# Optimization experiments

Hardware: AMD Instinct MI355X
Metric: run time of the kernel (lower is better)

The kernel has to match this reference:

```python
import jax, jax.numpy as jnp
import numpy as np

MAX_PAIRS = 130816  # = L*(L-1)//2 for L=512; matches init max_pairs


def setup_inputs() -> dict:
    key = jax.random.key(0)
    k1, k2, k3, k4, k5 = jax.random.split(key, 5)
    B, L, H = 32, 512, 1024
    hidden_states = jax.random.normal(k1, (B, L, H), dtype=jnp.float32)
    attention_mask = jax.random.randint(k2, (B, L), 0, 2, dtype=jnp.int32)
    special_tokens_mask = jax.random.randint(k3, (B, L), 0, 2, dtype=jnp.int32)
    # nn.Bilinear(H, H, 1): weight (1, H, H) -> squeeze to (H, H); bias (1,)
    bound = 1.0 / np.sqrt(H)
    W = jax.random.uniform(k4, (H, H), dtype=jnp.float32, minval=-bound, maxval=bound)
    b = jax.random.uniform(k5, (1,), dtype=jnp.float32, minval=-bound, maxval=bound)
    return {"hidden_states": hidden_states, "attention_mask": attention_mask,
            "special_tokens_mask": special_tokens_mask, "W": W, "b": b}


def reference(hidden_states, attention_mask, special_tokens_mask, W, b):
    # Dropout is identity in eval mode (reference assumes inference math).
    B, L, H = hidden_states.shape
    m = (attention_mask == 1) & (special_tokens_mask == 0)  # (B, L) valid AA positions

    # Bilinear score for every (t, s) pair: S[b,t,s] = h_t^T W h_s + bias
    u = jnp.einsum('blh,hk->blk', hidden_states, W)          # (B, L, H)
    S = jnp.einsum('blk,bmk->blm', u, hidden_states) + b[0]  # (B, L, L)

    # Compacted rank of each valid position (order-preserving, like nonzero()).
    r = jnp.cumsum(m.astype(jnp.int32), axis=-1) - 1          # (B, L)
    n = jnp.sum(m.astype(jnp.int32), axis=-1)[:, None, None]  # (B, 1, 1) = n_aa

    pos = jnp.arange(L, dtype=jnp.int32)
    # pair valid iff both positions are AA and t < s (compacted order preserves original order)
    valid = m[:, :, None] & m[:, None, :] & (pos[:, None] < pos[None, :])  # (B, L, L)

    i = r[:, :, None]  # compacted row index (B, L, 1)
    j = r[:, None, :]  # compacted col index (B, 1, L)
    # row-major upper-triangle (offset=1) linear index, matching torch.triu_indices order
    idx = i * (n - 1) - (i * (i - 1)) // 2 + (j - i - 1)
    idx = jnp.where(valid, idx, MAX_PAIRS)  # invalid pairs -> dump slot

    def scatter_one(s_row, ix_row):
        out = jnp.zeros((MAX_PAIRS + 1,), dtype=s_row.dtype)
        out = out.at[ix_row.reshape(-1)].set(s_row.reshape(-1))
        return out[:MAX_PAIRS]

    return jax.vmap(scatter_one)(S, idx)  # (B, MAX_PAIRS)
```

## Files before the change

### kernel.cpp

```cpp
#include <hip/hip_runtime.h>

constexpr int NB   = 32;
constexpr int LL   = 512;
constexpr int HH   = 1024;
constexpr int MAXP = 130816;
constexpr int RMAX = 256;

typedef __attribute__((ext_vector_type(8))) short short8;
typedef __attribute__((ext_vector_type(4))) float f32x4;

static __device__ inline unsigned short f2bf(float f) {
    unsigned int u = __float_as_uint(f);
    unsigned int r = (u + 0x7FFFu + ((u >> 16) & 1u)) >> 16;
    return (unsigned short)r;
}

#define GLOAD16(g, l) __builtin_amdgcn_global_load_lds( \
    (const __attribute__((address_space(1))) unsigned int*)(g), \
    (__attribute__((address_space(3))) unsigned int*)(l), 16, 0, 0)

__global__ __launch_bounds__(512) void prep1_kernel(
        const int* __restrict__ am, const int* __restrict__ sm,
        int* __restrict__ pos, int* __restrict__ ncnt,
        float4* __restrict__ out4, int n4) {
    if (blockIdx.x < NB) {
        int b = blockIdx.x;
        int t = threadIdx.x;
        bool m = (am[b * LL + t] == 1) && (sm[b * LL + t] == 0);
        unsigned long long bal = __ballot(m);
        int lane = t & 63;
        int w = t >> 6;
        __shared__ int wtot[8];
        if (lane == 0) wtot[w] = __popcll(bal);
        pos[b * LL + t] = 0;
        __syncthreads();
        int off = 0;
        for (int i = 0; i < w; ++i) off += wtot[i];
        int pre = __popcll(bal & ((1ULL << lane) - 1ULL));
        int r = off + pre;
        if (t == LL - 1) {
            int tot = 0;
            for (int i = 0; i < 8; ++i) tot += wtot[i];
            ncnt[b] = tot;
        }
        if (m) pos[b * LL + r] = t;
    } else {
        int i = (blockIdx.x - NB) * 512 + threadIdx.x;
        int stride = (gridDim.x - NB) * 512;
        float4 z = {0.f, 0.f, 0.f, 0.f};
        for (; i < n4; i += stride) out4[i] = z;
    }
}

__global__ __launch_bounds__(256) void prep2_kernel(
        const float* __restrict__ W, unsigned short* __restrict__ wt,
        const float* __restrict__ hs, const int* __restrict__ pos,
        const int* __restrict__ ncnt, unsigned short* __restrict__ hc) {
    if (blockIdx.x < 256) {
        __shared__ float T[64][65];
        int th = blockIdx.x >> 4, tj = blockIdx.x & 15;
        int t = threadIdx.x;
        int r0 = t >> 4, c4 = (t & 15) * 4;
        #pragma unroll
        for (int q = 0; q < 4; ++q) {
            int r = r0 + q * 16;
            float4 v = *(const float4*)(W + (size_t)(th * 64 + r) * HH + tj * 64 + c4);
            T[r][c4] = v.x; T[r][c4 + 1] = v.y; T[r][c4 + 2] = v.z; T[r][c4 + 3] = v.w;
        }
        __syncthreads();
        #pragma unroll
        for (int q = 0; q < 4; ++q) {
            int r = r0 + q * 16;
            ushort4 o;
            o.x = f2bf(T[c4 + 0][r]);
            o.y = f2bf(T[c4 + 1][r]);
            o.z = f2bf(T[c4 + 2][r]);
            o.w = f2bf(T[c4 + 3][r]);
            *(ushort4*)(wt + (size_t)(tj * 64 + r) * HH + th * 64 + c4) = o;
        }
    } else {
        int bi = blockIdx.x - 256;
        int b = bi >> 8, i = bi & 255;
        int n = min(ncnt[b], RMAX);
        int npad = min(RMAX, (n + 127) & ~127);
        if (i >= npad) return;
        int t = threadIdx.x;
        ushort4 o; o.x = 0; o.y = 0; o.z = 0; o.w = 0;
        if (i < n) {
            int g = pos[b * LL + i];
            float4 v = *(const float4*)(hs + ((size_t)b * LL + g) * HH + t * 4);
            o.x = f2bf(v.x); o.y = f2bf(v.y); o.z = f2bf(v.z); o.w = f2bf(v.w);
        }
        *(ushort4*)(hc + ((size_t)b * RMAX + i) * HH + t * 4) = o;
    }
}

__global__ __launch_bounds__(256) void gemm1_kernel(
        const unsigned short* __restrict__ hc, const unsigned short* __restrict__ wt,
        const int* __restrict__ ncnt, unsigned short* __restrict__ uc) {
    constexpr int BK = 64;
    int b = blockIdx.z;
    int n = min(ncnt[b], RMAX);
    int it = blockIdx.y;
    if (it * 64 >= n) return;
    int kt = blockIdx.x;

    __shared__ unsigned short As[64 * BK];
    __shared__ unsigned short Bs[64 * BK];

    int tid = threadIdx.x;
    int lane = tid & 63, w = tid >> 6, wr = w >> 1, wc = w & 1;

    const unsigned short* ga = hc + ((size_t)b * RMAX + it * 64) * HH;
    const unsigned short* gb = wt + (size_t)kt * 64 * HH;

    int f0 = tid, f1 = tid + 256;
    int r0 = f0 >> 3, r1 = f1 >> 3;
    int so0 = ((f0 & 7) ^ (r0 & 7)) * 8;
    int so1 = ((f1 & 7) ^ (r1 & 7)) * 8;

    f32x4 acc[2][2];
    #pragma unroll
    for (int m = 0; m < 2; ++m)
        #pragma unroll
        for (int nn = 0; nn < 2; ++nn) { acc[m][nn].x = 0.f; acc[m][nn].y = 0.f; acc[m][nn].z = 0.f; acc[m][nn].w = 0.f; }

    int fr = lane & 15;
    int khi = (lane >> 4) * 8;

    for (int k0 = 0; k0 < HH; k0 += BK) {
        GLOAD16(ga + (size_t)r0 * HH + k0 + so0, As + f0 * 8);
        GLOAD16(ga + (size_t)r1 * HH + k0 + so1, As + f1 * 8);
        GLOAD16(gb + (size_t)r0 * HH + k0 + so0, Bs + f0 * 8);
        GLOAD16(gb + (size_t)r1 * HH + k0 + so1, Bs + f1 * 8);
        __syncthreads();

        #pragma unroll
        for (int ks = 0; ks < 2; ++ks) {
            int k8 = ks * 32 + khi;
            short8 a[2], bb[2];
            #pragma unroll
            for (int m = 0; m < 2; ++m) {
                int row = wr * 32 + m * 16 + fr;
                a[m] = *(const short8*)&As[row * BK + (k8 ^ ((row & 7) * 8))];
            }
            #pragma unroll
            for (int nn = 0; nn < 2; ++nn) {
                int row = wc * 32 + nn * 16 + fr;
                bb[nn] = *(const short8*)&Bs[row * BK + (k8 ^ ((row & 7) * 8))];
            }
            #pragma unroll
            for (int m = 0; m < 2; ++m)
                #pragma unroll
                for (int nn = 0; nn < 2; ++nn)
                    acc[m][nn] = __builtin_amdgcn_mfma_f32_16x16x32_bf16(a[m], bb[nn], acc[m][nn], 0, 0, 0);
        }
        __syncthreads();
    }

    int rowb = it * 64 + wr * 32 + (lane >> 4) * 4;
    int colb = kt * 64 + wc * 32 + (lane & 15);
    #pragma unroll
    for (int m = 0; m < 2; ++m)
        #pragma unroll
        for (int nn = 0; nn < 2; ++nn)
            #pragma unroll
            for (int r = 0; r < 4; ++r)
                uc[((size_t)b * RMAX + rowb + m * 16 + r) * HH + colb + nn * 16] = f2bf(acc[m][nn][r]);
}

__global__ __launch_bounds__(256) void gemm2_kernel(
        const unsigned short* __restrict__ uc, const unsigned short* __restrict__ hc,
        const int* __restrict__ ncnt, const float* __restrict__ bias_p,
        float* __restrict__ out) {
    constexpr int BK = 64;
    int b = blockIdx.z;
    int it = blockIdx.y, jt = blockIdx.x;
    if (jt < it) return;
    int n = min(ncnt[b], RMAX);
    if (it * 64 >= n || jt * 64 >= n) return;

    __shared__ unsigned short Us[64 * BK];
    __shared__ unsigned short Hs[64 * BK];

    int tid = threadIdx.x;
    int lane = tid & 63, w = tid >> 6, wr = w >> 1, wc = w & 1;

    const unsigned short* ga = uc + ((size_t)b * RMAX + it * 64) * HH;
    const unsigned short* gb = hc + ((size_t)b * RMAX + jt * 64) * HH;

    int f0 = tid, f1 = tid + 256;
    int r0 = f0 >> 3, r1 = f1 >> 3;
    int so0 = ((f0 & 7) ^ (r0 & 7)) * 8;
    int so1 = ((f1 & 7) ^ (r1 & 7)) * 8;

    f32x4 acc[2][2];
    #pragma unroll
    for (int m = 0; m < 2; ++m)
        #pragma unroll
        for (int nn = 0; nn < 2; ++nn) { acc[m][nn].x = 0.f; acc[m][nn].y = 0.f; acc[m][nn].z = 0.f; acc[m][nn].w = 0.f; }

    int fr = lane & 15;
    int khi = (lane >> 4) * 8;

    for (int k0 = 0; k0 < HH; k0 += BK) {
        GLOAD16(ga + (size_t)r0 * HH + k0 + so0, Us + f0 * 8);
        GLOAD16(ga + (size_t)r1 * HH + k0 + so1, Us + f1 * 8);
        GLOAD16(gb + (size_t)r0 * HH + k0 + so0, Hs + f0 * 8);
        GLOAD16(gb + (size_t)r1 * HH + k0 + so1, Hs + f1 * 8);
        __syncthreads();

        #pragma unroll
        for (int ks = 0; ks < 2; ++ks) {
            int k8 = ks * 32 + khi;
            short8 a[2], bb[2];
            #pragma unroll
            for (int m = 0; m < 2; ++m) {
                int row = wr * 32 + m * 16 + fr;
                a[m] = *(const short8*)&Us[row * BK + (k8 ^ ((row & 7) * 8))];
            }
            #pragma unroll
            for (int nn = 0; nn < 2; ++nn) {
                int row = wc * 32 + nn * 16 + fr;
                bb[nn] = *(const short8*)&Hs[row * BK + (k8 ^ ((row & 7) * 8))];
            }
            #pragma unroll
            for (int m = 0; m < 2; ++m)
                #pragma unroll
                for (int nn = 0; nn < 2; ++nn)
                    acc[m][nn] = __builtin_amdgcn_mfma_f32_16x16x32_bf16(a[m], bb[nn], acc[m][nn], 0, 0, 0);
        }
        __syncthreads();
    }

    float bias = bias_p[0];
    #pragma unroll
    for (int m = 0; m < 2; ++m)
        #pragma unroll
        for (int nn = 0; nn < 2; ++nn)
            #pragma unroll
            for (int r = 0; r < 4; ++r) {
                int i = it * 64 + wr * 32 + m * 16 + (lane >> 4) * 4 + r;
                int j = jt * 64 + wc * 32 + nn * 16 + (lane & 15);
                if (i < j && j < n) {
                    int idx = i * (n - 1) - (i * (i - 1)) / 2 + (j - i - 1);
                    out[(size_t)b * MAXP + idx] = acc[m][nn][r] + bias;
                }
            }
}

extern "C" void kernel_launch(void* const* d_in, const int* in_sizes, int n_in,
                              void* d_out, int out_size, void* d_ws, size_t ws_size,
                              hipStream_t stream) {
    const float* hs  = (const float*)d_in[0];
    const int*   am  = (const int*)d_in[1];
    const int*   sm  = (const int*)d_in[2];
    const float* W   = (const float*)d_in[3];
    const float* bp  = (const float*)d_in[4];
    float* out = (float*)d_out;

    char* ws = (char*)d_ws;
    int* pos  = (int*)ws;
    int* ncnt = (int*)(ws + NB * LL * 4);
    unsigned short* hc = (unsigned short*)(ws + NB * LL * 4 + 256);
    unsigned short* wt = hc + (size_t)NB * RMAX * HH;
    unsigned short* uc = wt + (size_t)HH * HH;

    prep1_kernel<<<NB + 1024, 512, 0, stream>>>(am, sm, pos, ncnt,
                                                (float4*)out, (NB * MAXP) / 4);
    prep2_kernel<<<256 + NB * RMAX, 256, 0, stream>>>(W, wt, hs, pos, ncnt, hc);
    gemm1_kernel<<<dim3(HH / 64, RMAX / 64, NB), 256, 0, stream>>>(hc, wt, ncnt, uc);
    gemm2_kernel<<<dim3(RMAX / 64, RMAX / 64, NB), 256, 0, stream>>>(uc, hc, ncnt, bp, out);
}
```

Before: 56.65 us.

## Merge W transpose into prep kernel, widen gemm1 N-tile, trim gather padding

Moves the W transpose/bf16 conversion into the first prep kernel alongside mask compaction and output zeroing, and enlarges the zeroing grid. The gather becomes its own kernel with padding to multiples of 64 instead of 128, which skips some zero rows. gemm1 now uses a 64x128 tile with 8 accumulators per wave for more B reuse, and its grid order is swapped so the row tiles vary fastest. Address computation is hoisted out of the k-loops and f2bf is replaced with the library conversion. The larger tile raises register and LDS use, and the changed grid shape gives fewer blocks.

```diff
diff --git a/kernel.cpp b/kernel.cpp
--- a/kernel.cpp
+++ b/kernel.cpp
@@ -1,4 +1,5 @@
 #include <hip/hip_runtime.h>
+#include <hip/hip_bf16.h>
 
 constexpr int NB   = 32;
 constexpr int LL   = 512;
@@ -10,21 +11,23 @@
 typedef __attribute__((ext_vector_type(4))) float f32x4;
 
 static __device__ inline unsigned short f2bf(float f) {
-    unsigned int u = __float_as_uint(f);
-    unsigned int r = (u + 0x7FFFu + ((u >> 16) & 1u)) >> 16;
-    return (unsigned short)r;
+    __hip_bfloat16 h = __float2bfloat16(f);
+    union { __hip_bfloat16 h; unsigned short u; } cv; cv.h = h;
+    return cv.u;
 }
 
 #define GLOAD16(g, l) __builtin_amdgcn_global_load_lds( \
     (const __attribute__((address_space(1))) unsigned int*)(g), \
     (__attribute__((address_space(3))) unsigned int*)(l), 16, 0, 0)
 
-__global__ __launch_bounds__(512) void prep1_kernel(
+__global__ __launch_bounds__(512) void prep_kernel(
         const int* __restrict__ am, const int* __restrict__ sm,
         int* __restrict__ pos, int* __restrict__ ncnt,
+        const float* __restrict__ W, unsigned short* __restrict__ wt,
         float4* __restrict__ out4, int n4) {
-    if (blockIdx.x < NB) {
-        int b = blockIdx.x;
+    int bi = blockIdx.x;
+    if (bi < NB) {
+        int b = bi;
         int t = threadIdx.x;
         bool m = (am[b * LL + t] == 1) && (sm[b * LL + t] == 0);
         unsigned long long bal = __ballot(m);
@@ -44,55 +47,49 @@
             ncnt[b] = tot;
         }
         if (m) pos[b * LL + r] = t;
+    } else if (bi < NB + 256) {
+        __shared__ float T[64][65];
+        int tile = bi - NB;
+        int th = tile >> 4, tj = tile & 15;
+        int t = threadIdx.x;
+        int r = t >> 3;
+        int c8 = (t & 7) * 8;
+        float4 v0 = *(const float4*)(W + (size_t)(th * 64 + r) * HH + tj * 64 + c8);
+        float4 v1 = *(const float4*)(W + (size_t)(th * 64 + r) * HH + tj * 64 + c8 + 4);
+        T[r][c8 + 0] = v0.x; T[r][c8 + 1] = v0.y; T[r][c8 + 2] = v0.z; T[r][c8 + 3] = v0.w;
+        T[r][c8 + 4] = v1.x; T[r][c8 + 5] = v1.y; T[r][c8 + 6] = v1.z; T[r][c8 + 7] = v1.w;
+        __syncthreads();
+        ushort4 o0, o1;
+        o0.x = f2bf(T[c8 + 0][r]); o0.y = f2bf(T[c8 + 1][r]);
+        o0.z = f2bf(T[c8 + 2][r]); o0.w = f2bf(T[c8 + 3][r]);
+        o1.x = f2bf(T[c8 + 4][r]); o1.y = f2bf(T[c8 + 5][r]);
+        o1.z = f2bf(T[c8 + 6][r]); o1.w = f2bf(T[c8 + 7][r]);
+        unsigned short* dst = wt + (size_t)(tj * 64 + r) * HH + th * 64 + c8;
+        *(ushort4*)dst = o0;
+        *(ushort4*)(dst + 4) = o1;
     } else {
-        int i = (blockIdx.x - NB) * 512 + threadIdx.x;
-        int stride = (gridDim.x - NB) * 512;
+        int i = (bi - NB - 256) * 512 + threadIdx.x;
+        int stride = (gridDim.x - NB - 256) * 512;
         float4 z = {0.f, 0.f, 0.f, 0.f};
         for (; i < n4; i += stride) out4[i] = z;
     }
 }
 
-__global__ __launch_bounds__(256) void prep2_kernel(
-        const float* __restrict__ W, unsigned short* __restrict__ wt,
+__global__ __launch_bounds__(256) void gather_kernel(
         const float* __restrict__ hs, const int* __restrict__ pos,
         const int* __restrict__ ncnt, unsigned short* __restrict__ hc) {
-    if (blockIdx.x < 256) {
-        __shared__ float T[64][65];
-        int th = blockIdx.x >> 4, tj = blockIdx.x & 15;
-        int t = threadIdx.x;
-        int r0 = t >> 4, c4 = (t & 15) * 4;
-        #pragma unroll
-        for (int q = 0; q < 4; ++q) {
-            int r = r0 + q * 16;
-            float4 v = *(const float4*)(W + (size_t)(th * 64 + r) * HH + tj * 64 + c4);
-            T[r][c4] = v.x; T[r][c4 + 1] = v.y; T[r][c4 + 2] = v.z; T[r][c4 + 3] = v.w;
-        }
-        __syncthreads();
-        #pragma unroll
-        for (int q = 0; q < 4; ++q) {
-            int r = r0 + q * 16;
-            ushort4 o;
-            o.x = f2bf(T[c4 + 0][r]);
-            o.y = f2bf(T[c4 + 1][r]);
-            o.z = f2bf(T[c4 + 2][r]);
-            o.w = f2bf(T[c4 + 3][r]);
-            *(ushort4*)(wt + (size_t)(tj * 64 + r) * HH + th * 64 + c4) = o;
-        }
-    } else {
-        int bi = blockIdx.x - 256;
-        int b = bi >> 8, i = bi & 255;
-        int n = min(ncnt[b], RMAX);
-        int npad = min(RMAX, (n + 127) & ~127);
-        if (i >= npad) return;
-        int t = threadIdx.x;
-        ushort4 o; o.x = 0; o.y = 0; o.z = 0; o.w = 0;
-        if (i < n) {
-            int g = pos[b * LL + i];
-            float4 v = *(const float4*)(hs + ((size_t)b * LL + g) * HH + t * 4);
-            o.x = f2bf(v.x); o.y = f2bf(v.y); o.z = f2bf(v.z); o.w = f2bf(v.w);
-        }
-        *(ushort4*)(hc + ((size_t)b * RMAX + i) * HH + t * 4) = o;
-    }
+    int b = blockIdx.y, i = blockIdx.x;
+    int n = min(ncnt[b], RMAX);
+    int npad = min(RMAX, (n + 63) & ~63);
+    if (i >= npad) return;
+    int t = threadIdx.x;
+    ushort4 o; o.x = 0; o.y = 0; o.z = 0; o.w = 0;
+    if (i < n) {
+        int g = pos[b * LL + i];
+        float4 v = *(const float4*)(hs + ((size_t)b * LL + g) * HH + t * 4);
+        o.x = f2bf(v.x); o.y = f2bf(v.y); o.z = f2bf(v.z); o.w = f2bf(v.w);
+    }
+    *(ushort4*)(hc + ((size_t)b * RMAX + i) * HH + t * 4) = o;
 }
 
 __global__ __launch_bounds__(256) void gemm1_kernel(
@@ -101,69 +98,78 @@
     constexpr int BK = 64;
     int b = blockIdx.z;
     int n = min(ncnt[b], RMAX);
-    int it = blockIdx.y;
+    int it = blockIdx.x;
     if (it * 64 >= n) return;
-    int kt = blockIdx.x;
+    int kt = blockIdx.y;
 
     __shared__ unsigned short As[64 * BK];
-    __shared__ unsigned short Bs[64 * BK];
+    __shared__ unsigned short Bs[128 * BK];
 
     int tid = threadIdx.x;
     int lane = tid & 63, w = tid >> 6, wr = w >> 1, wc = w & 1;
 
     const unsigned short* ga = hc + ((size_t)b * RMAX + it * 64) * HH;
-    const unsigned short* gb = wt + (size_t)kt * 64 * HH;
-
-    int f0 = tid, f1 = tid + 256;
-    int r0 = f0 >> 3, r1 = f1 >> 3;
-    int so0 = ((f0 & 7) ^ (r0 & 7)) * 8;
-    int so1 = ((f1 & 7) ^ (r1 & 7)) * 8;
-
-    f32x4 acc[2][2];
-    #pragma unroll
-    for (int m = 0; m < 2; ++m)
-        #pragma unroll
-        for (int nn = 0; nn < 2; ++nn) { acc[m][nn].x = 0.f; acc[m][nn].y = 0.f; acc[m][nn].z = 0.f; acc[m][nn].w = 0.f; }
+    const unsigned short* gb = wt + (size_t)kt * 128 * HH;
+
+    int fa0 = tid, fa1 = tid + 256;
+    int ar0 = fa0 >> 3, ar1 = fa1 >> 3;
+    const unsigned short* gar0 = ga + (size_t)ar0 * HH + ((fa0 & 7) ^ (ar0 & 7)) * 8;
+    const unsigned short* gar1 = ga + (size_t)ar1 * HH + ((fa1 & 7) ^ (ar1 & 7)) * 8;
+    int fb0 = tid, fb1 = tid + 256, fb2 = tid + 512, fb3 = tid + 768;
+    int br0 = fb0 >> 3, br1 = fb1 >> 3, br2 = fb2 >> 3, br3 = fb3 >> 3;
+    const unsigned short* gbr0 = gb + (size_t)br0 * HH + ((fb0 & 7) ^ (br0 & 7)) * 8;
+    const unsigned short* gbr1 = gb + (size_t)br1 * HH + ((fb1 & 7) ^ (br1 & 7)) * 8;
+    const unsigned short* gbr2 = gb + (size_t)br2 * HH + ((fb2 & 7) ^ (br2 & 7)) * 8;
+    const unsigned short* gbr3 = gb + (size_t)br3 * HH + ((fb3 & 7) ^ (br3 & 7)) * 8;
+
+    f32x4 acc[2][4];
+    #pragma unroll
+    for (int m = 0; m < 2; ++m)
+        #pragma unroll
+        for (int nn = 0; nn < 4; ++nn) { acc[m][nn].x = 0.f; acc[m][nn].y = 0.f; acc[m][nn].z = 0.f; acc[m][nn].w = 0.f; }
 
     int fr = lane & 15;
     int khi = (lane >> 4) * 8;
 
     for (int k0 = 0; k0 < HH; k0 += BK) {
-        GLOAD16(ga + (size_t)r0 * HH + k0 + so0, As + f0 * 8);
-        GLOAD16(ga + (size_t)r1 * HH + k0 + so1, As + f1 * 8);
-        GLOAD16(gb + (size_t)r0 * HH + k0 + so0, Bs + f0 * 8);
-        GLOAD16(gb + (size_t)r1 * HH + k0 + so1, Bs + f1 * 8);
+        GLOAD16(gar0 + k0, As + fa0 * 8);
+        GLOAD16(gar1 + k0, As + fa1 * 8);
+        GLOAD16(gbr0 + k0, Bs + fb0 * 8);
+        GLOAD16(gbr1 + k0, Bs + fb1 * 8);
+        GLOAD16(gbr2 + k0, Bs + fb2 * 8);
+        GLOAD16(gbr3 + k0, Bs + fb3 * 8);
         __syncthreads();
 
         #pragma unroll
         for (int ks = 0; ks < 2; ++ks) {
             int k8 = ks * 32 + khi;
-            short8 a[2], bb[2];
-            #pragma unroll
-            for (int m = 0; m < 2; ++m) {
-                int row = wr * 32 + m * 16 + fr;
-                a[m] = *(const short8*)&As[row * BK + (k8 ^ ((row & 7) * 8))];
-            }
-            #pragma unroll
-            for (int nn = 0; nn < 2; ++nn) {
-                int row = wc * 32 + nn * 16 + fr;
+            short8 a0, a1, bb[4];
+            {
+                int row = wr * 32 + fr;
+                a0 = *(const short8*)&As[row * BK + (k8 ^ ((row & 7) * 8))];
+                row += 16;
+                a1 = *(const short8*)&As[row * BK + (k8 ^ ((row & 7) * 8))];
+            }
+            #pragma unroll
+            for (int nn = 0; nn < 4; ++nn) {
+                int row = wc * 64 + nn * 16 + fr;
                 bb[nn] = *(const short8*)&Bs[row * BK + (k8 ^ ((row & 7) * 8))];
             }
             #pragma unroll
-            for (int m = 0; m < 2; ++m)
-                #pragma unroll
-                for (int nn = 0; nn < 2; ++nn)
-                    acc[m][nn] = __builtin_amdgcn_mfma_f32_16x16x32_bf16(a[m], bb[nn], acc[m][nn], 0, 0, 0);
+            for (int nn = 0; nn < 4; ++nn) {
+                acc[0][nn] = __builtin_amdgcn_mfma_f32_16x16x32_bf16(a0, bb[nn], acc[0][nn], 0, 0, 0);
+                acc[1][nn] = __builtin_amdgcn_mfma_f32_16x16x32_bf16(a1, bb[nn], acc[1][nn], 0, 0, 0);
+            }
         }
         __syncthreads();
     }
 
     int rowb = it * 64 + wr * 32 + (lane >> 4) * 4;
-    int colb = kt * 64 + wc * 32 + (lane & 15);
-    #pragma unroll
-    for (int m = 0; m < 2; ++m)
-        #pragma unroll
-        for (int nn = 0; nn < 2; ++nn)
+    int colb = kt * 128 + wc * 64 + (lane & 15);
+    #pragma unroll
+    for (int m = 0; m < 2; ++m)
+        #pragma unroll
+        for (int nn = 0; nn < 4; ++nn)
             #pragma unroll
             for (int r = 0; r < 4; ++r)
                 uc[((size_t)b * RMAX + rowb + m * 16 + r) * HH + colb + nn * 16] = f2bf(acc[m][nn][r]);
@@ -191,8 +197,10 @@
 
     int f0 = tid, f1 = tid + 256;
     int r0 = f0 >> 3, r1 = f1 >> 3;
-    int so0 = ((f0 & 7) ^ (r0 & 7)) * 8;
-    int so1 = ((f1 & 7) ^ (r1 & 7)) * 8;
+    const unsigned short* gar0 = ga + (size_t)r0 * HH + ((f0 & 7) ^ (r0 & 7)) * 8;
+    const unsigned short* gar1 = ga + (size_t)r1 * HH + ((f1 & 7) ^ (r1 & 7)) * 8;
+    const unsigned short* gbr0 = gb + (size_t)r0 * HH + ((f0 & 7) ^ (r0 & 7)) * 8;
+    const unsigned short* gbr1 = gb + (size_t)r1 * HH + ((f1 & 7) ^ (r1 & 7)) * 8;
 
     f32x4 acc[2][2];
     #pragma unroll
@@ -204,31 +212,32 @@
     int khi = (lane >> 4) * 8;
 
     for (int k0 = 0; k0 < HH; k0 += BK) {
-        GLOAD16(ga + (size_t)r0 * HH + k0 + so0, Us + f0 * 8);
-        GLOAD16(ga + (size_t)r1 * HH + k0 + so1, Us + f1 * 8);
-        GLOAD16(gb + (size_t)r0 * HH + k0 + so0, Hs + f0 * 8);
-        GLOAD16(gb + (size_t)r1 * HH + k0 + so1, Hs + f1 * 8);
+        GLOAD16(gar0 + k0, Us + f0 * 8);
+        GLOAD16(gar1 + k0, Us + f1 * 8);
+        GLOAD16(gbr0 + k0, Hs + f0 * 8);
+        GLOAD16(gbr1 + k0, Hs + f1 * 8);
         __syncthreads();
 
         #pragma unroll
         for (int ks = 0; ks < 2; ++ks) {
             int k8 = ks * 32 + khi;
-            short8 a[2], bb[2];
-            #pragma unroll
-            for (int m = 0; m < 2; ++m) {
-                int row = wr * 32 + m * 16 + fr;
-                a[m] = *(const short8*)&Us[row * BK + (k8 ^ ((row & 7) * 8))];
-            }
-            #pragma unroll
-            for (int nn = 0; nn < 2; ++nn) {
-                int row = wc * 32 + nn * 16 + fr;
-                bb[nn] = *(const short8*)&Hs[row * BK + (k8 ^ ((row & 7) * 8))];
-            }
-            #pragma unroll
-            for (int m = 0; m < 2; ++m)
-                #pragma unroll
-                for (int nn = 0; nn < 2; ++nn)
-                    acc[m][nn] = __builtin_amdgcn_mfma_f32_16x16x32_bf16(a[m], bb[nn], acc[m][nn], 0, 0, 0);
+            short8 a0, a1, b0, b1;
+            {
+                int row = wr * 32 + fr;
+                a0 = *(const short8*)&Us[row * BK + (k8 ^ ((row & 7) * 8))];
+                row += 16;
+                a1 = *(const short8*)&Us[row * BK + (k8 ^ ((row & 7) * 8))];
+            }
+            {
+                int row = wc * 32 + fr;
+                b0 = *(const short8*)&Hs[row * BK + (k8 ^ ((row & 7) * 8))];
+                row += 16;
+                b1 = *(const short8*)&Hs[row * BK + (k8 ^ ((row & 7) * 8))];
+            }
+            acc[0][0] = __builtin_amdgcn_mfma_f32_16x16x32_bf16(a0, b0, acc[0][0], 0, 0, 0);
+            acc[0][1] = __builtin_amdgcn_mfma_f32_16x16x32_bf16(a0, b1, acc[0][1], 0, 0, 0);
+            acc[1][0] = __builtin_amdgcn_mfma_f32_16x16x32_bf16(a1, b0, acc[1][0], 0, 0, 0);
+            acc[1][1] = __builtin_amdgcn_mfma_f32_16x16x32_bf16(a1, b1, acc[1][1], 0, 0, 0);
         }
         __syncthreads();
     }
@@ -262,13 +271,14 @@
     char* ws = (char*)d_ws;
     int* pos  = (int*)ws;
     int* ncnt = (int*)(ws + NB * LL * 4);
-    unsigned short* hc = (unsigned short*)(ws + NB * LL * 4 + 256);
-    unsigned short* wt = hc + (size_t)NB * RMAX * HH;
-    unsigned short* uc = wt + (size_t)HH * HH;
-
-    prep1_kernel<<<NB + 1024, 512, 0, stream>>>(am, sm, pos, ncnt,
-                                                (float4*)out, (NB * MAXP) / 4);
-    prep2_kernel<<<256 + NB * RMAX, 256, 0, stream>>>(W, wt, hs, pos, ncnt, hc);
-    gemm1_kernel<<<dim3(HH / 64, RMAX / 64, NB), 256, 0, stream>>>(hc, wt, ncnt, uc);
+    unsigned short* wt = (unsigned short*)(ws + NB * LL * 4 + 256);
+    unsigned short* hc = wt + (size_t)HH * HH;
+    unsigned short* uc = hc + (size_t)NB * RMAX * HH;
+
+    int n4 = (NB * MAXP) / 4;
+    prep_kernel<<<NB + 256 + 2016, 512, 0, stream>>>(am, sm, pos, ncnt, W, wt,
+                                                     (float4*)out, n4);
+    gather_kernel<<<dim3(RMAX, NB), 256, 0, stream>>>(hs, pos, ncnt, hc);
+    gemm1_kernel<<<dim3(RMAX / 64, HH / 128, NB), 256, 0, stream>>>(hc, wt, ncnt, uc);
     gemm2_kernel<<<dim3(RMAX / 64, RMAX / 64, NB), 256, 0, stream>>>(uc, hc, ncnt, bp, out);
 }
```

Result: faster. 51.02 us (-9.9%).
